# Performance work log

Hardware: AMD Instinct MI355X
Metric: run time of the kernel (lower is better)

The kernel has to match this reference:

```python
import jax, jax.numpy as jnp
import numpy as np

EPS = 1e-6

def feature_map(x):
    # 'elu' feature map: elu(x) + 1 (positive feature map from Katharopoulos et al.)
    return jax.nn.elu(x) + 1.0

def setup_inputs() -> dict:
    key = jax.random.key(0)
    kq, kk, kv = jax.random.split(key, 3)
    B, L, H, D = 4, 2048, 16, 64
    q = jax.random.normal(kq, (B, L, H, D), dtype=jnp.float32)
    k = jax.random.normal(kk, (B, L, H, D), dtype=jnp.float32)
    v = jax.random.normal(kv, (B, L, H, D), dtype=jnp.float32)
    return {"q": q, "k": k, "v": v}

def reference(q, k, v):
    # q, k, v: [N, L, H, D]  (attention_mask=None -> causal linear attention)
    qf = feature_map(q)
    kf = feature_map(k)
    # normalizer: z[n,l,h] = sum_d qf[n,l,h,d] * cumsum_s<=l kf[n,s,h,d]
    z = jnp.einsum('nlhd,nlhd->nlh', qf, jnp.cumsum(kf, axis=1)) + EPS
    # causal_dot_product via scan over sequence with carry S[n,h,d,m]
    B, L, H, D = q.shape
    M = v.shape[-1]
    qs = jnp.moveaxis(qf, 1, 0)  # [L, N, H, D]
    ks = jnp.moveaxis(kf, 1, 0)
    vs = jnp.moveaxis(v, 1, 0)

    def step(S, qkv):
        ql, kl, vl = qkv                              # [N,H,D], [N,H,D], [N,H,M]
        S = S + jnp.einsum('nhd,nhm->nhdm', kl, vl)   # running sum of k v^T
        out = jnp.einsum('nhd,nhdm->nhm', ql, S)
        return S, out

    S0 = jnp.zeros((B, H, D, M), dtype=q.dtype)
    _, outs = jax.lax.scan(step, S0, (qs, ks, vs))    # outs: [L, N, H, M]
    v_ = jnp.moveaxis(outs, 0, 1)                     # [N, L, H, M]
    return v_ / z[..., None]
```

## Files before the change

kernel.cpp:

```cpp
#include <hip/hip_runtime.h>
#include <cstdint>

#define LL 2048
#define HH 16
#define DD 64
#define NC 32
#define LSTR 1024
#define EPSF 1e-6f
#define PAD 72

typedef __bf16 bf16x8 __attribute__((ext_vector_type(8)));
typedef float floatx4 __attribute__((ext_vector_type(4)));
typedef unsigned short ushortx8 __attribute__((ext_vector_type(8)));
typedef unsigned short ushortx4 __attribute__((ext_vector_type(4)));
typedef unsigned short ushortx2 __attribute__((ext_vector_type(2)));

static __device__ __forceinline__ float fmap(float x){ return x > 0.f ? x + 1.f : __expf(x); }
static __device__ __forceinline__ unsigned short f2bf(float f){
    unsigned u = __builtin_bit_cast(unsigned, f);
    u += 0x7fffu + ((u >> 16) & 1u);
    return (unsigned short)(u >> 16);
}
static __device__ __forceinline__ float bf2f(unsigned short s){
    unsigned u = ((unsigned)s) << 16;
    return __builtin_bit_cast(float, u);
}
static __device__ __forceinline__ bf16x8 ldf(const unsigned short* p){
    return __builtin_bit_cast(bf16x8, *(const ushortx8*)p);
}

__global__ __launch_bounds__(256) void k1(const float* __restrict__ kp, const float* __restrict__ vp,
                                          unsigned short* __restrict__ kvt, float* __restrict__ ks)
{
    __shared__ __align__(16) unsigned short kft[DD*PAD];
    __shared__ __align__(16) unsigned short v_s[DD*PAD];
    const int ci = blockIdx.x;
    const int c = ci & 31, bh = ci >> 5, b = bh >> 4, h = bh & 15;
    const int t = threadIdx.x;
    const int64_t gbase = ((int64_t)(b*LL + c*DD)*HH + h)*DD;
#pragma unroll
    for (int i = 0; i < 2; ++i) {
        int flat = t + 256*i;
        int l0 = (flat >> 4) * 2, col = (flat & 15) << 2;
        const float* g0 = kp + gbase + (int64_t)l0*LSTR + col;
        float4 ka = *(const float4*)(g0);
        float4 kb = *(const float4*)(g0 + LSTR);
        unsigned short ua[4] = { f2bf(fmap(ka.x)), f2bf(fmap(ka.y)), f2bf(fmap(ka.z)), f2bf(fmap(ka.w)) };
        unsigned short ub[4] = { f2bf(fmap(kb.x)), f2bf(fmap(kb.y)), f2bf(fmap(kb.z)), f2bf(fmap(kb.w)) };
#pragma unroll
        for (int e = 0; e < 4; ++e)
            *(ushortx2*)(kft + (col+e)*PAD + l0) = ushortx2{ ua[e], ub[e] };
        const float* v0 = vp + gbase + (int64_t)l0*LSTR + col;
        float4 va = *(const float4*)(v0);
        float4 vb = *(const float4*)(v0 + LSTR);
        *(ushortx4*)(v_s + l0*PAD + col)     = ushortx4{ f2bf(va.x), f2bf(va.y), f2bf(va.z), f2bf(va.w) };
        *(ushortx4*)(v_s + (l0+1)*PAD + col) = ushortx4{ f2bf(vb.x), f2bf(vb.y), f2bf(vb.z), f2bf(vb.w) };
    }
    __syncthreads();
    const int w = t >> 6, lane = t & 63, quad = lane >> 4, lr = lane & 15;
    const int m0 = 16*w;
    floatx4 acc[4];
#pragma unroll
    for (int dt = 0; dt < 4; ++dt) acc[dt] = floatx4{0.f,0.f,0.f,0.f};
#pragma unroll
    for (int kk = 0; kk < 2; ++kk) {
        ushortx8 u;
#pragma unroll
        for (int j = 0; j < 8; ++j)
            u[j] = v_s[(kk*32 + quad*8 + j)*PAD + m0 + lr];
        bf16x8 a = __builtin_bit_cast(bf16x8, u);
#pragma unroll
        for (int dt = 0; dt < 4; ++dt) {
            bf16x8 bb = ldf(kft + (dt*16+lr)*PAD + kk*32 + quad*8);
            acc[dt] = __builtin_amdgcn_mfma_f32_16x16x32_bf16(a, bb, acc[dt], 0, 0, 0);
        }
    }
    unsigned short* kvo = kvt + (int64_t)ci*4096;
#pragma unroll
    for (int dt = 0; dt < 4; ++dt)
#pragma unroll
        for (int r = 0; r < 4; ++r)
            kvo[(m0 + quad*4 + r)*DD + dt*16 + lr] = f2bf(acc[dt][r]);
    if (t < DD) {
        float s = 0.f;
#pragma unroll
        for (int j = 0; j < 8; ++j) {
            ushortx8 u = *(const ushortx8*)(kft + t*PAD + j*8);
#pragma unroll
            for (int e = 0; e < 8; ++e) s += bf2f(u[e]);
        }
        ks[(int64_t)ci*DD + t] = s;
    }
}

__global__ __launch_bounds__(256) void k2(unsigned short* __restrict__ kvt, float* __restrict__ ks)
{
    const int blk = blockIdx.x;
    const int bh = blk >> 3, part = blk & 7, t = threadIdx.x;
    unsigned short* base = kvt + (int64_t)bh*NC*4096 + (part*256 + t)*2;
    float r0 = 0.f, r1 = 0.f;
    unsigned x = *(const unsigned*)base;
    for (int c = 0; c < NC-1; ++c) {
        unsigned xn = *(const unsigned*)(base + (int64_t)(c+1)*4096);
        unsigned o = (unsigned)f2bf(r0) | ((unsigned)f2bf(r1) << 16);
        r0 += bf2f((unsigned short)(x & 0xffffu));
        r1 += bf2f((unsigned short)(x >> 16));
        *(unsigned*)(base + (int64_t)c*4096) = o;
        x = xn;
    }
    *(unsigned*)(base + (int64_t)(NC-1)*4096) = (unsigned)f2bf(r0) | ((unsigned)f2bf(r1) << 16);
    if (part == 0 && t < DD) {
        float r = 0.f;
        float* kb = ks + (int64_t)bh*NC*DD + t;
        for (int c = 0; c < NC; ++c) { float xx = kb[(int64_t)c*DD]; kb[(int64_t)c*DD] = r; r += xx; }
    }
}

__global__ __launch_bounds__(256) void k3(const float* __restrict__ qp, const float* __restrict__ kp,
                                          const float* __restrict__ vp,
                                          const unsigned short* __restrict__ kvt,
                                          const float* __restrict__ ks, float* __restrict__ outp)
{
    __shared__ __align__(16) unsigned short kfx[80*PAD];
    __shared__ __align__(16) unsigned short v_s[DD*PAD];
    __shared__ float zr[DD];
    const int ci = blockIdx.x;
    const int c = ci & 31, bh = ci >> 5, b = bh >> 4, h = bh & 15;
    const int t = threadIdx.x;
    const int64_t gbase = ((int64_t)(b*LL + c*DD)*HH + h)*DD;
    const unsigned short* kvg = kvt + (int64_t)ci*4096;
    const float* ksg = ks + (int64_t)ci*DD;
#pragma unroll
    for (int i = 0; i < 4; ++i) {
        int flat = t + 256*i;
        int l = flat >> 4, col = (flat & 15) << 2;
        float4 kq = *(const float4*)(kp + gbase + (int64_t)l*LSTR + col);
        float4 vq = *(const float4*)(vp + gbase + (int64_t)l*LSTR + col);
        *(ushortx4*)(kfx + l*PAD + col) = ushortx4{ f2bf(fmap(kq.x)), f2bf(fmap(kq.y)), f2bf(fmap(kq.z)), f2bf(fmap(kq.w)) };
        *(ushortx4*)(v_s + l*PAD + col) = ushortx4{ f2bf(vq.x), f2bf(vq.y), f2bf(vq.z), f2bf(vq.w) };
    }
    if (t < 135) *(ushortx8*)(kfx + 65*PAD + t*8) = ushortx8{0,0,0,0,0,0,0,0};
    if (t < DD)  kfx[64*PAD + t] = f2bf(ksg[t]);

    const int w = t >> 6, lane = t & 63, quad = lane >> 4, lr = lane & 15;
    const int l0 = 16*w;
    bf16x8 aq[2];
#pragma unroll
    for (int kk = 0; kk < 2; ++kk) {
        const float* g = qp + gbase + (int64_t)(l0+lr)*LSTR + kk*32 + quad*8;
        float4 x0 = *(const float4*)(g);
        float4 x1 = *(const float4*)(g + 4);
        ushortx8 u = { f2bf(fmap(x0.x)), f2bf(fmap(x0.y)), f2bf(fmap(x0.z)), f2bf(fmap(x0.w)),
                       f2bf(fmap(x1.x)), f2bf(fmap(x1.y)), f2bf(fmap(x1.z)), f2bf(fmap(x1.w)) };
        aq[kk] = __builtin_bit_cast(bf16x8, u);
    }
    __syncthreads();

    floatx4 sc[5];
#pragma unroll
    for (int tt = 0; tt < 5; ++tt) sc[tt] = floatx4{0.f,0.f,0.f,0.f};
#pragma unroll
    for (int kk = 0; kk < 2; ++kk)
#pragma unroll
        for (int tt = 0; tt < 5; ++tt) {
            bf16x8 bb = ldf(kfx + (tt*16+lr)*PAD + kk*32 + quad*8);
            sc[tt] = __builtin_amdgcn_mfma_f32_16x16x32_bf16(aq[kk], bb, sc[tt], 0, 0, 0);
        }
    __syncthreads();

    float zp[4] = {0.f,0.f,0.f,0.f};
#pragma unroll
    for (int tt = 0; tt < 4; ++tt)
#pragma unroll
        for (int r = 0; r < 4; ++r) {
            int row = l0 + quad*4 + r;
            int col = tt*16 + lr;
            float val = (col <= row) ? sc[tt][r] : 0.f;
            zp[r] += val;
            kfx[row*PAD + col] = f2bf(val);
        }
#pragma unroll
    for (int r = 0; r < 4; ++r) zp[r] += (lr == 0) ? sc[4][r] : 0.f;
#pragma unroll
    for (int m = 1; m < 16; m <<= 1)
#pragma unroll
        for (int r = 0; r < 4; ++r) zp[r] += __shfl_xor(zp[r], m, 64);
    if (lr == 0)
#pragma unroll
        for (int r = 0; r < 4; ++r) zr[l0 + quad*4 + r] = 1.f / (zp[r] + EPSF);

    floatx4 oa[4];
#pragma unroll
    for (int mt = 0; mt < 4; ++mt) oa[mt] = floatx4{0.f,0.f,0.f,0.f};
#pragma unroll
    for (int kk = 0; kk < 2; ++kk) {
        bf16x8 a2 = ldf(kfx + (l0+lr)*PAD + kk*32 + quad*8);
#pragma unroll
        for (int mt = 0; mt < 4; ++mt) {
            ushortx8 uv;
#pragma unroll
            for (int j = 0; j < 8; ++j)
                uv[j] = v_s[(kk*32 + quad*8 + j)*PAD + mt*16 + lr];
            bf16x8 bv = __builtin_bit_cast(bf16x8, uv);
            oa[mt] = __builtin_amdgcn_mfma_f32_16x16x32_bf16(a2, bv, oa[mt], 0, 0, 0);
        }
    }
#pragma unroll
    for (int kk = 0; kk < 2; ++kk)
#pragma unroll
        for (int mt = 0; mt < 4; ++mt) {
            bf16x8 bs = ldf(kvg + (mt*16+lr)*64 + kk*32 + quad*8);
            oa[mt] = __builtin_amdgcn_mfma_f32_16x16x32_bf16(aq[kk], bs, oa[mt], 0, 0, 0);
        }
#pragma unroll
    for (int r = 0; r < 4; ++r) {
        int row = l0 + quad*4 + r;
        float rz = zr[row];
#pragma unroll
        for (int mt = 0; mt < 4; ++mt)
            outp[gbase + (int64_t)row*LSTR + mt*16 + lr] = oa[mt][r] * rz;
    }
}

extern "C" void kernel_launch(void* const* d_in, const int* in_sizes, int n_in,
                              void* d_out, int out_size, void* d_ws, size_t ws_size,
                              hipStream_t stream) {
    const float* q = (const float*)d_in[0];
    const float* k = (const float*)d_in[1];
    const float* v = (const float*)d_in[2];
    float* out = (float*)d_out;
    unsigned short* kvt = (unsigned short*)d_ws;
    float* ks = (float*)((char*)d_ws + (size_t)2048*4096*2);
    k1<<<2048, 256, 0, stream>>>(k, v, kvt, ks);
    k2<<<512,  256, 0, stream>>>(kvt, ks);
    k3<<<2048, 256, 0, stream>>>(q, k, v, kvt, ks, out);
}
```

Baseline: 157.7 us.

## Store V transposed in LDS and stage Q through shared memory

Both kernels now write V into LDS transposed (dimension-major), so the MFMA operand becomes one 16-byte vector load instead of eight scalar strided LDS reads. In k3, Q is loaded cooperatively with coalesced float4 reads into its own LDS tile and its feature map is computed there. The masked score tile is written into that tile, which removes the second barrier. The KV-state operands are prefetched from global memory early so their latency overlaps the score computation. In exchange, LDS use per block grows, which may reduce occupancy, and the transposed 2-element stores may cause bank conflicts.

Measured after the change: 156.0 us. About the same (-1.1%).

```diff
diff --git a/kernel.cpp b/kernel.cpp
--- a/kernel.cpp
+++ b/kernel.cpp
@@ -33,7 +33,7 @@
                                           unsigned short* __restrict__ kvt, float* __restrict__ ks)
 {
     __shared__ __align__(16) unsigned short kft[DD*PAD];
-    __shared__ __align__(16) unsigned short v_s[DD*PAD];
+    __shared__ __align__(16) unsigned short vtt[DD*PAD];
     const int ci = blockIdx.x;
     const int c = ci & 31, bh = ci >> 5, b = bh >> 4, h = bh & 15;
     const int t = threadIdx.x;
@@ -42,19 +42,19 @@
     for (int i = 0; i < 2; ++i) {
         int flat = t + 256*i;
         int l0 = (flat >> 4) * 2, col = (flat & 15) << 2;
-        const float* g0 = kp + gbase + (int64_t)l0*LSTR + col;
-        float4 ka = *(const float4*)(g0);
-        float4 kb = *(const float4*)(g0 + LSTR);
-        unsigned short ua[4] = { f2bf(fmap(ka.x)), f2bf(fmap(ka.y)), f2bf(fmap(ka.z)), f2bf(fmap(ka.w)) };
-        unsigned short ub[4] = { f2bf(fmap(kb.x)), f2bf(fmap(kb.y)), f2bf(fmap(kb.z)), f2bf(fmap(kb.w)) };
-#pragma unroll
-        for (int e = 0; e < 4; ++e)
-            *(ushortx2*)(kft + (col+e)*PAD + l0) = ushortx2{ ua[e], ub[e] };
-        const float* v0 = vp + gbase + (int64_t)l0*LSTR + col;
-        float4 va = *(const float4*)(v0);
-        float4 vb = *(const float4*)(v0 + LSTR);
-        *(ushortx4*)(v_s + l0*PAD + col)     = ushortx4{ f2bf(va.x), f2bf(va.y), f2bf(va.z), f2bf(va.w) };
-        *(ushortx4*)(v_s + (l0+1)*PAD + col) = ushortx4{ f2bf(vb.x), f2bf(vb.y), f2bf(vb.z), f2bf(vb.w) };
+        const float* gk = kp + gbase + (int64_t)l0*LSTR + col;
+        const float* gv = vp + gbase + (int64_t)l0*LSTR + col;
+        float4 ka = *(const float4*)(gk);
+        float4 kb = *(const float4*)(gk + LSTR);
+        float4 va = *(const float4*)(gv);
+        float4 vb = *(const float4*)(gv + LSTR);
+        float kaa[4] = {ka.x,ka.y,ka.z,ka.w}, kbb[4] = {kb.x,kb.y,kb.z,kb.w};
+        float vaa[4] = {va.x,va.y,va.z,va.w}, vbb[4] = {vb.x,vb.y,vb.z,vb.w};
+#pragma unroll
+        for (int e = 0; e < 4; ++e) {
+            *(ushortx2*)(kft + (col+e)*PAD + l0) = ushortx2{ f2bf(fmap(kaa[e])), f2bf(fmap(kbb[e])) };
+            *(ushortx2*)(vtt + (col+e)*PAD + l0) = ushortx2{ f2bf(vaa[e]), f2bf(vbb[e]) };
+        }
     }
     __syncthreads();
     const int w = t >> 6, lane = t & 63, quad = lane >> 4, lr = lane & 15;
@@ -64,11 +64,7 @@
     for (int dt = 0; dt < 4; ++dt) acc[dt] = floatx4{0.f,0.f,0.f,0.f};
 #pragma unroll
     for (int kk = 0; kk < 2; ++kk) {
-        ushortx8 u;
-#pragma unroll
-        for (int j = 0; j < 8; ++j)
-            u[j] = v_s[(kk*32 + quad*8 + j)*PAD + m0 + lr];
-        bf16x8 a = __builtin_bit_cast(bf16x8, u);
+        bf16x8 a = ldf(vtt + (m0+lr)*PAD + kk*32 + quad*8);
 #pragma unroll
         for (int dt = 0; dt < 4; ++dt) {
             bf16x8 bb = ldf(kft + (dt*16+lr)*PAD + kk*32 + quad*8);
@@ -121,8 +117,9 @@
                                           const unsigned short* __restrict__ kvt,
                                           const float* __restrict__ ks, float* __restrict__ outp)
 {
+    __shared__ __align__(16) unsigned short qf [DD*PAD];
     __shared__ __align__(16) unsigned short kfx[80*PAD];
-    __shared__ __align__(16) unsigned short v_s[DD*PAD];
+    __shared__ __align__(16) unsigned short vtt[DD*PAD];
     __shared__ float zr[DD];
     const int ci = blockIdx.x;
     const int c = ci & 31, bh = ci >> 5, b = bh >> 4, h = bh & 15;
@@ -131,30 +128,42 @@
     const unsigned short* kvg = kvt + (int64_t)ci*4096;
     const float* ksg = ks + (int64_t)ci*DD;
 #pragma unroll
-    for (int i = 0; i < 4; ++i) {
+    for (int i = 0; i < 2; ++i) {
         int flat = t + 256*i;
-        int l = flat >> 4, col = (flat & 15) << 2;
-        float4 kq = *(const float4*)(kp + gbase + (int64_t)l*LSTR + col);
-        float4 vq = *(const float4*)(vp + gbase + (int64_t)l*LSTR + col);
-        *(ushortx4*)(kfx + l*PAD + col) = ushortx4{ f2bf(fmap(kq.x)), f2bf(fmap(kq.y)), f2bf(fmap(kq.z)), f2bf(fmap(kq.w)) };
-        *(ushortx4*)(v_s + l*PAD + col) = ushortx4{ f2bf(vq.x), f2bf(vq.y), f2bf(vq.z), f2bf(vq.w) };
+        int l0 = (flat >> 4) * 2, col = (flat & 15) << 2;
+        const float* gq = qp + gbase + (int64_t)l0*LSTR + col;
+        const float* gk = kp + gbase + (int64_t)l0*LSTR + col;
+        const float* gv = vp + gbase + (int64_t)l0*LSTR + col;
+        float4 qa = *(const float4*)(gq);
+        float4 qb = *(const float4*)(gq + LSTR);
+        float4 ka = *(const float4*)(gk);
+        float4 kb = *(const float4*)(gk + LSTR);
+        float4 va = *(const float4*)(gv);
+        float4 vb = *(const float4*)(gv + LSTR);
+        *(ushortx4*)(qf + l0*PAD + col)      = ushortx4{ f2bf(fmap(qa.x)), f2bf(fmap(qa.y)), f2bf(fmap(qa.z)), f2bf(fmap(qa.w)) };
+        *(ushortx4*)(qf + (l0+1)*PAD + col)  = ushortx4{ f2bf(fmap(qb.x)), f2bf(fmap(qb.y)), f2bf(fmap(qb.z)), f2bf(fmap(qb.w)) };
+        *(ushortx4*)(kfx + l0*PAD + col)     = ushortx4{ f2bf(fmap(ka.x)), f2bf(fmap(ka.y)), f2bf(fmap(ka.z)), f2bf(fmap(ka.w)) };
+        *(ushortx4*)(kfx + (l0+1)*PAD + col) = ushortx4{ f2bf(fmap(kb.x)), f2bf(fmap(kb.y)), f2bf(fmap(kb.z)), f2bf(fmap(kb.w)) };
+        float vaa[4] = {va.x,va.y,va.z,va.w}, vbb[4] = {vb.x,vb.y,vb.z,vb.w};
+#pragma unroll
+        for (int e = 0; e < 4; ++e)
+            *(ushortx2*)(vtt + (col+e)*PAD + l0) = ushortx2{ f2bf(vaa[e]), f2bf(vbb[e]) };
     }
     if (t < 135) *(ushortx8*)(kfx + 65*PAD + t*8) = ushortx8{0,0,0,0,0,0,0,0};
     if (t < DD)  kfx[64*PAD + t] = f2bf(ksg[t]);
+    __syncthreads();
 
     const int w = t >> 6, lane = t & 63, quad = lane >> 4, lr = lane & 15;
     const int l0 = 16*w;
     bf16x8 aq[2];
-#pragma unroll
-    for (int kk = 0; kk < 2; ++kk) {
-        const float* g = qp + gbase + (int64_t)(l0+lr)*LSTR + kk*32 + quad*8;
-        float4 x0 = *(const float4*)(g);
-        float4 x1 = *(const float4*)(g + 4);
-        ushortx8 u = { f2bf(fmap(x0.x)), f2bf(fmap(x0.y)), f2bf(fmap(x0.z)), f2bf(fmap(x0.w)),
-                       f2bf(fmap(x1.x)), f2bf(fmap(x1.y)), f2bf(fmap(x1.z)), f2bf(fmap(x1.w)) };
-        aq[kk] = __builtin_bit_cast(bf16x8, u);
-    }
-    __syncthreads();
+    aq[0] = ldf(qf + (l0+lr)*PAD + quad*8);
+    aq[1] = ldf(qf + (l0+lr)*PAD + 32 + quad*8);
+    bf16x8 bs[2][4];
+#pragma unroll
+    for (int kk = 0; kk < 2; ++kk)
+#pragma unroll
+        for (int mt = 0; mt < 4; ++mt)
+            bs[kk][mt] = ldf(kvg + (mt*16+lr)*DD + kk*32 + quad*8);
 
     floatx4 sc[5];
 #pragma unroll
@@ -166,7 +175,6 @@
             bf16x8 bb = ldf(kfx + (tt*16+lr)*PAD + kk*32 + quad*8);
             sc[tt] = __builtin_amdgcn_mfma_f32_16x16x32_bf16(aq[kk], bb, sc[tt], 0, 0, 0);
         }
-    __syncthreads();
 
     float zp[4] = {0.f,0.f,0.f,0.f};
 #pragma unroll
@@ -177,7 +185,7 @@
             int col = tt*16 + lr;
             float val = (col <= row) ? sc[tt][r] : 0.f;
             zp[r] += val;
-            kfx[row*PAD + col] = f2bf(val);
+            qf[row*PAD + col] = f2bf(val);
         }
 #pragma unroll
     for (int r = 0; r < 4; ++r) zp[r] += (lr == 0) ? sc[4][r] : 0.f;
@@ -194,24 +202,18 @@
     for (int mt = 0; mt < 4; ++mt) oa[mt] = floatx4{0.f,0.f,0.f,0.f};
 #pragma unroll
     for (int kk = 0; kk < 2; ++kk) {
-        bf16x8 a2 = ldf(kfx + (l0+lr)*PAD + kk*32 + quad*8);
+        bf16x8 a2 = ldf(qf + (l0+lr)*PAD + kk*32 + quad*8);
 #pragma unroll
         for (int mt = 0; mt < 4; ++mt) {
-            ushortx8 uv;
-#pragma unroll
-            for (int j = 0; j < 8; ++j)
-                uv[j] = v_s[(kk*32 + quad*8 + j)*PAD + mt*16 + lr];
-            bf16x8 bv = __builtin_bit_cast(bf16x8, uv);
+            bf16x8 bv = ldf(vtt + (mt*16+lr)*PAD + kk*32 + quad*8);
             oa[mt] = __builtin_amdgcn_mfma_f32_16x16x32_bf16(a2, bv, oa[mt], 0, 0, 0);
         }
     }
 #pragma unroll
     for (int kk = 0; kk < 2; ++kk)
 #pragma unroll
-        for (int mt = 0; mt < 4; ++mt) {
-            bf16x8 bs = ldf(kvg + (mt*16+lr)*64 + kk*32 + quad*8);
-            oa[mt] = __builtin_amdgcn_mfma_f32_16x16x32_bf16(aq[kk], bs, oa[mt], 0, 0, 0);
-        }
+        for (int mt = 0; mt < 4; ++mt)
+            oa[mt] = __builtin_amdgcn_mfma_f32_16x16x32_bf16(aq[kk], bs[kk][mt], oa[mt], 0, 0, 0);
 #pragma unroll
     for (int r = 0; r < 4; ++r) {
         int row = l0 + quad*4 + r;
```
